# Kernel tuning notes

Hardware: AMD Instinct MI355X
Metric: run time of the kernel (lower is better)

The kernel has to match this reference:

```python
import jax, jax.numpy as jnp
import numpy as np

B, S, D, Q, U = 32, 8192, 256, 256, 128


def setup_inputs() -> dict:
    key = jax.random.key(0)
    k1, k2, k3, k4, k5 = jax.random.split(key, 5)
    query = jax.random.normal(k1, (B, Q), dtype=jnp.float32)
    values = jax.random.normal(k2, (B, S, D), dtype=jnp.float32)
    # Dense kernels (Keras stores as [in, out]); scale ~ Glorot-ish
    W1 = jax.random.normal(k3, (D, U), dtype=jnp.float32) * 0.05
    W2 = jax.random.normal(k4, (Q, U), dtype=jnp.float32) * 0.05
    V = jax.random.normal(k5, (U, 1), dtype=jnp.float32) * 0.05
    return {"query": query, "values": values, "W1": W1, "W2": W2, "V": V}


def reference(query, values, W1, W2, V):
    # score = V^T tanh(W1*values + W2*query)  -> (B, S, 1)
    proj_v = jnp.einsum('bsd,du->bsu', values, W1)          # (B,S,U)
    proj_q = jnp.einsum('bq,qu->bu', query, W2)[:, None, :]  # (B,1,U)
    score = jnp.einsum('bsu,uo->bso', jnp.tanh(proj_v + proj_q), V)  # (B,S,1)
    attention_weights = jax.nn.softmax(score, axis=1)        # softmax over seq_len
    # dropout is identity at inference (training=False)
    context = jnp.sum(attention_weights * values, axis=1)    # (B,D)
    return context, attention_weights
```

## Files before the change

### kernel.cpp

```cpp
#include <hip/hip_runtime.h>
#include <stdint.h>

#define B_ 32
#define S_ 8192
#define D_ 256
#define Q_ 256
#define U_ 128
#define NCHUNK 64

typedef float floatx4 __attribute__((ext_vector_type(4)));
typedef float f32x4 __attribute__((ext_vector_type(4)));
typedef __bf16 bf16x8 __attribute__((ext_vector_type(8)));
typedef unsigned short ushortx4 __attribute__((ext_vector_type(4)));

static __device__ __forceinline__ unsigned short f2bf(float f) {
    unsigned int x = __builtin_bit_cast(unsigned int, f);
    x += 0x7FFFu + ((x >> 16) & 1u);
    return (unsigned short)(x >> 16);
}

static __device__ __forceinline__ float fast_tanh(float x) {
    x = fminf(15.f, fmaxf(-15.f, x));
    float e = __expf(2.f * x);
    return __fdividef(e - 1.f, e + 1.f);
}

__global__ __launch_bounds__(128) void prep_kernel(
        const float* __restrict__ query, const float* __restrict__ W1,
        const float* __restrict__ W2, float* __restrict__ pq,
        unsigned short* __restrict__ w1t) {
    int b = blockIdx.x;
    int t = threadIdx.x;
    __shared__ float qrow[Q_];
    qrow[t] = query[b * Q_ + t];
    qrow[t + 128] = query[b * Q_ + 128 + t];
    __syncthreads();
    float acc = 0.f;
#pragma unroll 8
    for (int q = 0; q < Q_; ++q) acc = fmaf(qrow[q], W2[q * U_ + t], acc);
    pq[b * U_ + t] = acc;
    int base = (b * 128 + t) * 8;
#pragma unroll
    for (int j = 0; j < 8; ++j) {
        int e = base + j;
        int n = e >> 8, k = e & 255;
        w1t[e] = f2bf(W1[k * U_ + n]);
    }
}

__global__ __launch_bounds__(256) void fused_kernel(
        const float* __restrict__ values, const unsigned short* __restrict__ w1t,
        const float* __restrict__ pq, const float* __restrict__ V,
        float* __restrict__ scores, float* __restrict__ mbuf,
        float* __restrict__ lbuf, float* __restrict__ cpart) {
    __shared__ unsigned short As[128 * 40];
    __shared__ unsigned short Bs[128 * 40];
    __shared__ float part[256];
    __shared__ float sarr[128];
    __shared__ float parr[128];
    __shared__ float redm[1];
    __shared__ floatx4 cbuf[256];

    int b = blockIdx.y;
    int cid = blockIdx.x;
    int s0 = cid * 128;
    int tid = threadIdx.x;
    int lane = tid & 63;
    int wave = tid >> 6;
    int wr = wave >> 1, wc = wave & 1;
    int cc = lane & 15, qg = lane >> 4;

    const float* vb = values + ((size_t)b * S_ + s0) * D_;

    f32x4 acc[4][4];
#pragma unroll
    for (int mt = 0; mt < 4; ++mt)
#pragma unroll
        for (int nt = 0; nt < 4; ++nt) acc[mt][nt] = (f32x4){0.f, 0.f, 0.f, 0.f};

    for (int kt = 0; kt < 8; ++kt) {
        int k0 = kt * 32;
        __syncthreads();
#pragma unroll
        for (int i = 0; i < 4; ++i) {
            int idx = tid + i * 256;
            int row = idx >> 3, c = idx & 7;
            floatx4 v = *reinterpret_cast<const floatx4*>(vb + (size_t)row * D_ + k0 + c * 4);
            ushortx4 u;
            u[0] = f2bf(v[0]); u[1] = f2bf(v[1]); u[2] = f2bf(v[2]); u[3] = f2bf(v[3]);
            *reinterpret_cast<ushortx4*>(&As[row * 40 + c * 4]) = u;
            ushortx4 w = *reinterpret_cast<const ushortx4*>(&w1t[row * 256 + k0 + c * 4]);
            *reinterpret_cast<ushortx4*>(&Bs[row * 40 + c * 4]) = w;
        }
        __syncthreads();
        bf16x8 af[4], bfr[4];
#pragma unroll
        for (int mt = 0; mt < 4; ++mt)
            af[mt] = *reinterpret_cast<const bf16x8*>(&As[(wr * 64 + mt * 16 + cc) * 40 + qg * 8]);
#pragma unroll
        for (int nt = 0; nt < 4; ++nt)
            bfr[nt] = *reinterpret_cast<const bf16x8*>(&Bs[(wc * 64 + nt * 16 + cc) * 40 + qg * 8]);
#pragma unroll
        for (int mt = 0; mt < 4; ++mt)
#pragma unroll
            for (int nt = 0; nt < 4; ++nt)
                acc[mt][nt] = __builtin_amdgcn_mfma_f32_16x16x32_bf16(af[mt], bfr[nt], acc[mt][nt], 0, 0, 0);
    }

    float Vu[4], pqu[4];
#pragma unroll
    for (int nt = 0; nt < 4; ++nt) {
        int u = wc * 64 + nt * 16 + cc;
        Vu[nt] = V[u];
        pqu[nt] = pq[b * U_ + u];
    }
#pragma unroll
    for (int mt = 0; mt < 4; ++mt) {
#pragma unroll
        for (int r = 0; r < 4; ++r) {
            float s = 0.f;
#pragma unroll
            for (int nt = 0; nt < 4; ++nt)
                s += Vu[nt] * fast_tanh(acc[mt][nt][r] + pqu[nt]);
            s += __shfl_xor(s, 1);
            s += __shfl_xor(s, 2);
            s += __shfl_xor(s, 4);
            s += __shfl_xor(s, 8);
            if (cc == 0) part[wc * 128 + wr * 64 + mt * 16 + qg * 4 + r] = s;
        }
    }
    __syncthreads();
    if (tid < 128) {
        float sc = part[tid] + part[128 + tid];
        scores[(size_t)b * S_ + s0 + tid] = sc;
        sarr[tid] = sc;
    }
    __syncthreads();
    if (tid < 64) {
        float m = fmaxf(sarr[tid], sarr[tid + 64]);
#pragma unroll
        for (int off = 32; off >= 1; off >>= 1) m = fmaxf(m, __shfl_xor(m, off));
        if (tid == 0) redm[0] = m;
    }
    __syncthreads();
    float M = redm[0];
    if (tid < 128) parr[tid] = __expf(sarr[tid] - M);
    __syncthreads();
    if (tid < 64) {
        float l = parr[tid] + parr[tid + 64];
#pragma unroll
        for (int off = 32; off >= 1; off >>= 1) l += __shfl_xor(l, off);
        if (tid == 0) { mbuf[b * NCHUNK + cid] = M; lbuf[b * NCHUNK + cid] = l; }
    }

    int g = tid & 63, sub = tid >> 6;
    floatx4 acc4 = {0.f, 0.f, 0.f, 0.f};
#pragma unroll 4
    for (int i = 0; i < 32; ++i) {
        int r = i * 4 + sub;
        float w = parr[r];
        floatx4 v = *reinterpret_cast<const floatx4*>(vb + (size_t)r * D_ + g * 4);
        acc4 += v * w;
    }
    cbuf[tid] = acc4;
    __syncthreads();
    if (tid < 64) {
        floatx4 r4 = cbuf[tid] + cbuf[tid + 64] + cbuf[tid + 128] + cbuf[tid + 192];
        *reinterpret_cast<floatx4*>(cpart + ((size_t)b * NCHUNK + cid) * D_ + g * 4) = r4;
    }
}

__global__ __launch_bounds__(256) void finalize_kernel(
        const float* __restrict__ scores, const float* __restrict__ mbuf,
        const float* __restrict__ lbuf, const float* __restrict__ cpart,
        float* __restrict__ out) {
    int b = blockIdx.x;
    int tid = threadIdx.x;
    __shared__ float alpha[NCHUNK];
    __shared__ float MZ[2];
    if (tid < 64) {
        float m = mbuf[b * NCHUNK + tid];
        float l = lbuf[b * NCHUNK + tid];
        float M = m;
#pragma unroll
        for (int off = 32; off >= 1; off >>= 1) M = fmaxf(M, __shfl_xor(M, off));
        float z = l * __expf(m - M);
#pragma unroll
        for (int off = 32; off >= 1; off >>= 1) z += __shfl_xor(z, off);
        if (tid == 0) { MZ[0] = M; MZ[1] = z; }
    }
    __syncthreads();
    float M = MZ[0];
    float invZ = 1.f / MZ[1];
    if (tid < 64) alpha[tid] = __expf(mbuf[b * NCHUNK + tid] - M) * invZ;
    __syncthreads();

    const floatx4* sc4 = reinterpret_cast<const floatx4*>(scores + (size_t)b * S_);
    floatx4* w4 = reinterpret_cast<floatx4*>(out + B_ * D_ + (size_t)b * S_);
#pragma unroll
    for (int i = 0; i < 8; ++i) {
        floatx4 v = sc4[tid + i * 256];
        floatx4 w;
#pragma unroll
        for (int j = 0; j < 4; ++j) w[j] = __expf(v[j] - M) * invZ;
        w4[tid + i * 256] = w;
    }

    float acc = 0.f;
#pragma unroll 8
    for (int c = 0; c < NCHUNK; ++c)
        acc = fmaf(alpha[c], cpart[((size_t)b * NCHUNK + c) * D_ + tid], acc);
    out[b * D_ + tid] = acc;
}

extern "C" void kernel_launch(void* const* d_in, const int* in_sizes, int n_in,
                              void* d_out, int out_size, void* d_ws, size_t ws_size,
                              hipStream_t stream) {
    const float* query  = (const float*)d_in[0];
    const float* values = (const float*)d_in[1];
    const float* W1     = (const float*)d_in[2];
    const float* W2     = (const float*)d_in[3];
    const float* V      = (const float*)d_in[4];
    float* out = (float*)d_out;

    char* ws = (char*)d_ws;
    unsigned short* w1t = (unsigned short*)ws;               ws += 65536;
    float* pq     = (float*)ws;                              ws += 16384;
    float* scores = (float*)ws;                              ws += B_ * S_ * 4;
    float* mbuf   = (float*)ws;                              ws += B_ * NCHUNK * 4;
    float* lbuf   = (float*)ws;                              ws += B_ * NCHUNK * 4;
    float* cpart  = (float*)ws;

    prep_kernel<<<dim3(32), dim3(128), 0, stream>>>(query, W1, W2, pq, w1t);
    fused_kernel<<<dim3(NCHUNK, B_), dim3(256), 0, stream>>>(values, w1t, pq, V,
                                                             scores, mbuf, lbuf, cpart);
    finalize_kernel<<<dim3(B_), dim3(256), 0, stream>>>(scores, mbuf, lbuf, cpart, out);
}
```

Measured before the change: 428.5 us.

## Widen K tile to 64, alias shared memory, and split finalize across blocks

The fused kernel now stages 64-wide K slices (four iterations instead of eight) using wider 8-element loads for W1, with a padded row stride of 72. The shared-memory buffers are aliased into one region, and launch bounds request four blocks per CU, to cut the barrier count and raise occupancy. The finalize kernel now launches a grid of (B, 9): eight blocks per batch write the normalized weights in parallel, and a ninth combines the partial contexts. This adds parallelism to a kernel that previously ran only 32 blocks. In exchange, each 9-block group recomputes the global max and sum, and the launch-bounds hint may push the compiler toward register spills.

```diff
diff --git a/kernel.cpp b/kernel.cpp
--- a/kernel.cpp
+++ b/kernel.cpp
@@ -7,11 +7,13 @@
 #define Q_ 256
 #define U_ 128
 #define NCHUNK 64
+#define LSTR 72
 
 typedef float floatx4 __attribute__((ext_vector_type(4)));
 typedef float f32x4 __attribute__((ext_vector_type(4)));
 typedef __bf16 bf16x8 __attribute__((ext_vector_type(8)));
 typedef unsigned short ushortx4 __attribute__((ext_vector_type(4)));
+typedef unsigned short ushortx8 __attribute__((ext_vector_type(8)));
 
 static __device__ __forceinline__ unsigned short f2bf(float f) {
     unsigned int x = __builtin_bit_cast(unsigned int, f);
@@ -48,18 +50,19 @@
     }
 }
 
-__global__ __launch_bounds__(256) void fused_kernel(
+__global__ __launch_bounds__(256, 4) void fused_kernel(
         const float* __restrict__ values, const unsigned short* __restrict__ w1t,
         const float* __restrict__ pq, const float* __restrict__ V,
         float* __restrict__ scores, float* __restrict__ mbuf,
         float* __restrict__ lbuf, float* __restrict__ cpart) {
-    __shared__ unsigned short As[128 * 40];
-    __shared__ unsigned short Bs[128 * 40];
-    __shared__ float part[256];
-    __shared__ float sarr[128];
-    __shared__ float parr[128];
-    __shared__ float redm[1];
-    __shared__ floatx4 cbuf[256];
+    __shared__ __align__(16) char smem[2 * 128 * LSTR * 2];
+    unsigned short* As = (unsigned short*)smem;
+    unsigned short* Bs = As + 128 * LSTR;
+    float* part = (float*)smem;
+    float* sarr = part + 256;
+    float* parr = sarr + 128;
+    float* redm = parr + 128;
+    floatx4* cbuf = (floatx4*)(smem + 4096);
 
     int b = blockIdx.y;
     int cid = blockIdx.x;
@@ -78,34 +81,47 @@
 #pragma unroll
         for (int nt = 0; nt < 4; ++nt) acc[mt][nt] = (f32x4){0.f, 0.f, 0.f, 0.f};
 
-    for (int kt = 0; kt < 8; ++kt) {
-        int k0 = kt * 32;
+    int arow = tid >> 4, ac = tid & 15;
+    int brow = tid >> 3, bc = tid & 7;
+
+    for (int kt = 0; kt < 4; ++kt) {
+        int k0 = kt * 64;
         __syncthreads();
 #pragma unroll
-        for (int i = 0; i < 4; ++i) {
-            int idx = tid + i * 256;
-            int row = idx >> 3, c = idx & 7;
-            floatx4 v = *reinterpret_cast<const floatx4*>(vb + (size_t)row * D_ + k0 + c * 4);
+        for (int i = 0; i < 8; ++i) {
+            int row = arow + i * 16;
+            floatx4 v = *reinterpret_cast<const floatx4*>(vb + (size_t)row * D_ + k0 + ac * 4);
             ushortx4 u;
             u[0] = f2bf(v[0]); u[1] = f2bf(v[1]); u[2] = f2bf(v[2]); u[3] = f2bf(v[3]);
-            *reinterpret_cast<ushortx4*>(&As[row * 40 + c * 4]) = u;
-            ushortx4 w = *reinterpret_cast<const ushortx4*>(&w1t[row * 256 + k0 + c * 4]);
-            *reinterpret_cast<ushortx4*>(&Bs[row * 40 + c * 4]) = w;
+            *reinterpret_cast<ushortx4*>(&As[row * LSTR + ac * 4]) = u;
+        }
+#pragma unroll
+        for (int i = 0; i < 4; ++i) {
+            int row = brow + i * 32;
+            ushortx8 w = *reinterpret_cast<const ushortx8*>(&w1t[row * 256 + k0 + bc * 8]);
+            *reinterpret_cast<ushortx8*>(&Bs[row * LSTR + bc * 8]) = w;
         }
         __syncthreads();
-        bf16x8 af[4], bfr[4];
-#pragma unroll
-        for (int mt = 0; mt < 4; ++mt)
-            af[mt] = *reinterpret_cast<const bf16x8*>(&As[(wr * 64 + mt * 16 + cc) * 40 + qg * 8]);
-#pragma unroll
-        for (int nt = 0; nt < 4; ++nt)
-            bfr[nt] = *reinterpret_cast<const bf16x8*>(&Bs[(wc * 64 + nt * 16 + cc) * 40 + qg * 8]);
-#pragma unroll
-        for (int mt = 0; mt < 4; ++mt)
+#pragma unroll
+        for (int ks = 0; ks < 2; ++ks) {
+            bf16x8 af[4], bfr[4];
+#pragma unroll
+            for (int mt = 0; mt < 4; ++mt)
+                af[mt] = *reinterpret_cast<const bf16x8*>(
+                    &As[(wr * 64 + mt * 16 + cc) * LSTR + ks * 32 + qg * 8]);
 #pragma unroll
             for (int nt = 0; nt < 4; ++nt)
-                acc[mt][nt] = __builtin_amdgcn_mfma_f32_16x16x32_bf16(af[mt], bfr[nt], acc[mt][nt], 0, 0, 0);
-    }
+                bfr[nt] = *reinterpret_cast<const bf16x8*>(
+                    &Bs[(wc * 64 + nt * 16 + cc) * LSTR + ks * 32 + qg * 8]);
+#pragma unroll
+            for (int mt = 0; mt < 4; ++mt)
+#pragma unroll
+                for (int nt = 0; nt < 4; ++nt)
+                    acc[mt][nt] = __builtin_amdgcn_mfma_f32_16x16x32_bf16(
+                        af[mt], bfr[nt], acc[mt][nt], 0, 0, 0);
+        }
+    }
+    __syncthreads();
 
     float Vu[4], pqu[4];
 #pragma unroll
@@ -175,9 +191,10 @@
         const float* __restrict__ lbuf, const float* __restrict__ cpart,
         float* __restrict__ out) {
     int b = blockIdx.x;
+    int part_id = blockIdx.y;
     int tid = threadIdx.x;
+    __shared__ float MZ[2];
     __shared__ float alpha[NCHUNK];
-    __shared__ float MZ[2];
     if (tid < 64) {
         float m = mbuf[b * NCHUNK + tid];
         float l = lbuf[b * NCHUNK + tid];
@@ -192,25 +209,23 @@
     __syncthreads();
     float M = MZ[0];
     float invZ = 1.f / MZ[1];
-    if (tid < 64) alpha[tid] = __expf(mbuf[b * NCHUNK + tid] - M) * invZ;
-    __syncthreads();
-
-    const floatx4* sc4 = reinterpret_cast<const floatx4*>(scores + (size_t)b * S_);
-    floatx4* w4 = reinterpret_cast<floatx4*>(out + B_ * D_ + (size_t)b * S_);
-#pragma unroll
-    for (int i = 0; i < 8; ++i) {
-        floatx4 v = sc4[tid + i * 256];
+
+    if (part_id < 8) {
+        size_t off = (size_t)b * S_ + part_id * 1024;
+        floatx4 v = *reinterpret_cast<const floatx4*>(scores + off + tid * 4);
         floatx4 w;
 #pragma unroll
         for (int j = 0; j < 4; ++j) w[j] = __expf(v[j] - M) * invZ;
-        w4[tid + i * 256] = w;
-    }
-
-    float acc = 0.f;
+        *reinterpret_cast<floatx4*>(out + B_ * D_ + off + tid * 4) = w;
+    } else {
+        if (tid < 64) alpha[tid] = __expf(mbuf[b * NCHUNK + tid] - M) * invZ;
+        __syncthreads();
+        float acc = 0.f;
 #pragma unroll 8
-    for (int c = 0; c < NCHUNK; ++c)
-        acc = fmaf(alpha[c], cpart[((size_t)b * NCHUNK + c) * D_ + tid], acc);
-    out[b * D_ + tid] = acc;
+        for (int c = 0; c < NCHUNK; ++c)
+            acc = fmaf(alpha[c], cpart[((size_t)b * NCHUNK + c) * D_ + tid], acc);
+        out[b * D_ + tid] = acc;
+    }
 }
 
 extern "C" void kernel_launch(void* const* d_in, const int* in_sizes, int n_in,
@@ -234,5 +249,5 @@
     prep_kernel<<<dim3(32), dim3(128), 0, stream>>>(query, W1, W2, pq, w1t);
     fused_kernel<<<dim3(NCHUNK, B_), dim3(256), 0, stream>>>(values, w1t, pq, V,
                                                              scores, mbuf, lbuf, cpart);
-    finalize_kernel<<<dim3(B_), dim3(256), 0, stream>>>(scores, mbuf, lbuf, cpart, out);
-}
+    finalize_kernel<<<dim3(B_, 9), dim3(256), 0, stream>>>(scores, mbuf, lbuf, cpart, out);
+}
```

New measurement: 419.3 us. 1.02x faster.
